# Kernel tuning notes

Hardware: AMD Instinct MI355X
Metric: run time of the kernel (lower is better)

## Reference

```python
import jax, jax.numpy as jnp
import numpy as np

# ---- constants from the source module ----
N_SAMPLES = 2 ** 15          # exp.n_samples
N_FRAMES = 128
N_HARMONICS = 8
N_EVENTS = 8
FILT_SIZE = 16               # freq_domain_filter_size
N_NOTES = 128                # len(scale)
NYQ = 22050.0 / 2.0          # samplerate nyquist
MIN_F0 = 40.0 / NYQ
F0_SPAN = (3000.0 / NYQ) - MIN_F0
MIN_RES = 0.5
RES_SPAN = 1.0 - MIN_RES
B_EVENTS = 128               # batch(16) * n_events(8)

# packed layout (build_param_slices order):
SL_F0 = slice(0, N_NOTES)                       # 0:128
SL_AMP = slice(N_NOTES + N_FRAMES, N_NOTES + 2 * N_FRAMES)   # 256:384
SL_HAMP = slice(N_NOTES + 2 * N_FRAMES, N_NOTES + 2 * N_FRAMES + N_HARMONICS)  # 384:392
SL_HDEC = slice(N_NOTES + 2 * N_FRAMES + N_HARMONICS, N_NOTES + 2 * N_FRAMES + 2 * N_HARMONICS)  # 392:400
SL_FENV = slice(N_NOTES + 2 * N_FRAMES + 2 * N_HARMONICS, N_NOTES + 2 * N_FRAMES + 2 * N_HARMONICS + FILT_SIZE)  # 400:416


def interp_linear(x, out_size):
    """F.interpolate(..., mode='linear', align_corners=False) on last dim of [B,C,L]."""
    L = x.shape[-1]
    scale = L / out_size
    coords = (jnp.arange(out_size, dtype=x.dtype) + 0.5) * scale - 0.5
    coords = jnp.clip(coords, 0.0, L - 1)
    i0 = jnp.floor(coords).astype(jnp.int32)
    i1 = jnp.minimum(i0 + 1, L - 1)
    w = coords - i0.astype(x.dtype)
    return x[..., i0] * (1.0 - w) + x[..., i1] * w


def setup_inputs() -> dict:
    key = jax.random.key(0)
    k1, k2 = jax.random.split(key)
    packed = jax.random.uniform(k1, (B_EVENTS, N_NOTES + 2 * N_FRAMES + 2 * N_HARMONICS + FILT_SIZE), dtype=jnp.float32)
    # musical-scale center frequencies, normalized by nyquist (geometric 20..3000 Hz)
    hz = 20.0 * (3000.0 / 20.0) ** (np.arange(N_NOTES) / (N_NOTES - 1))
    frequencies = jnp.asarray(hz / NYQ, dtype=jnp.float32)
    global_amp = jnp.full((1,), 5000.0, dtype=jnp.float32)
    osc_amp = jnp.full((1,), 50.0, dtype=jnp.float32)
    noise = jax.random.uniform(k2, (B_EVENTS, 1, N_SAMPLES), dtype=jnp.float32, minval=-1.0, maxval=1.0)
    return {"packed": packed, "frequencies": frequencies, "global_amp": global_amp,
            "osc_amp": osc_amp, "noise": noise}


def reference(packed, frequencies, global_amp, osc_amp, noise):
    B = packed.shape[0]
    # ---- f0 (discrete): softmax over notes, expectation, squared, repeated per frame ----
    f0_scalar = jax.nn.softmax(packed[:, SL_F0], axis=-1) @ frequencies          # [B]
    f0 = (f0_scalar ** 2)[:, None, None] * jnp.ones((1, 1, N_FRAMES), packed.dtype)  # [B,1,F]
    f0 = f0 * NYQ
    f0 = MIN_F0 + f0 * F0_SPAN
    # (the torch line `f0 + f0 + f0_fine` has no assignment -> no effect; f0_fine unused)

    # ---- oscillator bank ----
    harm_factors = jnp.arange(1, N_HARMONICS + 1, dtype=packed.dtype)
    osc = f0 * harm_factors[None, :, None]                      # [B,H,F]
    radians = osc / NYQ * jnp.pi
    radians = jnp.where(radians >= jnp.pi, 0.0, radians)
    radians = interp_linear(radians, N_SAMPLES)                  # [B,H,S]
    osc_bank = jnp.sin(jnp.cumsum(radians, axis=-1)) * osc_amp   # [B,H,S]

    # ---- per-harmonic amplitude recurrence (scan over frames) ----
    harm_decay = MIN_RES + packed[:, SL_HDEC] * RES_SPAN         # [B,H]
    harm_amp = packed[:, SL_HAMP]                                # [B,H]
    amp = packed[:, SL_AMP][:, None, :] * 2.0 - 1.0              # [B,1,F]

    def step(current, amp_i):                                    # current [B,H], amp_i [B,1]
        cur = jnp.maximum(current + amp_i * harm_amp, 0.0)       # clamp(0, inf)
        return cur * harm_decay, cur

    amp_frames = jnp.moveaxis(amp[:, 0, :], 1, 0)[:, :, None]    # [F,B,1]
    _, res = jax.lax.scan(step, jnp.zeros((B, N_HARMONICS), packed.dtype), amp_frames)
    res = jnp.moveaxis(res, 0, 2)                                # [B,H,F]
    res_full = interp_linear(res, N_SAMPLES)                     # [B,H,S]

    # ---- FFT-filtered noise ----
    amp_full = interp_linear(amp, N_SAMPLES)                     # [B,1,S]
    nf = packed[:, SL_FENV][:, None, :]                          # [B,1,16]
    nf = interp_linear(nf, N_SAMPLES // 2)
    nf = jnp.pad(nf, ((0, 0), (0, 0), (0, 1)))                   # [B,1,S//2+1]
    noise_scaled = noise * global_amp
    spec = jnp.fft.rfft(noise_scaled, axis=-1, norm='ortho')
    filt = spec * nf
    noise_out = jnp.fft.irfft(filt, n=N_SAMPLES, axis=-1, norm='ortho')
    noise_out = noise_out * jnp.where(amp_full >= 0, amp_full, 0.2 * amp_full)  # leaky_relu(0.2)

    # ---- combine ----
    x = res_full * osc_bank                                      # [B,H,S]
    x = noise_out / N_HARMONICS + x                              # broadcast [B,1,S]
    x = x.reshape(-1, N_EVENTS, N_HARMONICS, N_SAMPLES)
    x = jnp.sum(x, axis=(1, 2)).reshape(-1, 1, N_SAMPLES)        # [batch,1,S]
    return x
```

## Files before the change

### kernel.cpp

```cpp
#include <hip/hip_runtime.h>
#include <math.h>

#define PCK_STRIDE 416
#define N_SAMPLES  32768
#define FFT_M      16384
#define B_EVENTS   128
#define N_GROUPS   16
#define PI_F 3.14159265358979323846f
#define RT2H 0.70710678118654752f

#define MAP(i) ((i) + (((i) >> 5) << 2))
#define LDS_N  18432

__device__ inline float filt_at(const float* __restrict__ f, int k) {
    if (k >= FFT_M) return 0.0f;
    float c = ((float)k + 0.5f) * (1.0f / 1024.0f) - 0.5f;
    c = fminf(fmaxf(c, 0.0f), 15.0f);
    int i0 = (int)floorf(c);
    int i1 = min(i0 + 1, 15);
    float w = c - (float)i0;
    return f[i0] * (1.0f - w) + f[i1] * w;
}

__global__ __launch_bounds__(128) void prep_kernel(
    const float* __restrict__ packed, const float* __restrict__ freqs,
    float* __restrict__ rW, float* __restrict__ res)
{
    const int b = blockIdx.x;
    const int t = threadIdx.x;
    __shared__ float sm[128];
    __shared__ float s_amp[128];
    const float* row = packed + b * PCK_STRIDE;
    float lv = row[t];
    s_amp[t] = row[256 + t] * 2.0f - 1.0f;
    sm[t] = lv; __syncthreads();
    for (int s = 64; s > 0; s >>= 1) { if (t < s) sm[t] = fmaxf(sm[t], sm[t + s]); __syncthreads(); }
    float mx = sm[0]; __syncthreads();
    float ex = __expf(lv - mx);
    sm[t] = ex; __syncthreads();
    for (int s = 64; s > 0; s >>= 1) { if (t < s) sm[t] += sm[t + s]; __syncthreads(); }
    float den = sm[0]; __syncthreads();
    sm[t] = ex * freqs[t]; __syncthreads();
    for (int s = 64; s > 0; s >>= 1) { if (t < s) sm[t] += sm[t + s]; __syncthreads(); }
    float num = sm[0];

    if (t < 8) {
        const float MIN_F0 = 40.0f / 11025.0f;
        const float F0_SPAN = 3000.0f / 11025.0f - 40.0f / 11025.0f;
        float f0s = num / den;
        float f0 = MIN_F0 + f0s * f0s * 11025.0f * F0_SPAN;
        float r = f0 * (float)(t + 1) * (PI_F / 11025.0f);
        if (r >= PI_F) r = 0.0f;
        rW[b * 8 + t] = r;
        float ha = row[384 + t];
        float hd = 0.5f + row[392 + t] * 0.5f;
        float cur = 0.0f;
        float* rr = res + (b * 8 + t) * 128;
        for (int f = 0; f < 128; ++f) {
            float c = fmaxf(cur + s_amp[f] * ha, 0.0f);
            rr[f] = c;
            cur = c * hd;
        }
    }
}

template<int L>
__device__ inline void r4_dif_stage(float* re, float* im, int tid) {
    constexpr int q = L >> 2;
    constexpr float ang = -6.28318530717958647692f / (float)L;
    #pragma unroll 2
    for (int s = 0; s < 8; ++s) {
        int m = tid + (s << 9);
        int t = m & (q - 1);
        int i0 = ((m & ~(q - 1)) << 2) | t;
        int ia = MAP(i0), ib = MAP(i0 + q), ic = MAP(i0 + 2 * q), id = MAP(i0 + 3 * q);
        float ar = re[ia], ai = im[ia];
        float br = re[ib], bi = im[ib];
        float cr = re[ic], ci = im[ic];
        float dr = re[id], di = im[id];
        float s1, c1; __sincosf(ang * (float)t, &s1, &c1);
        float c2 = c1 * c1 - s1 * s1, s2 = 2.0f * c1 * s1;
        float c3 = c2 * c1 - s2 * s1, s3 = c2 * s1 + s2 * c1;
        float s0r = ar + cr, s0i = ai + ci;
        float t1r = br + dr, t1i = bi + di;
        float d0r = ar - cr, d0i = ai - ci;
        float d1r = br - dr, d1i = bi - di;
        re[ia] = s0r + t1r; im[ia] = s0i + t1i;
        float er = s0r - t1r, ei = s0i - t1i;
        re[ib] = er * c2 - ei * s2; im[ib] = er * s2 + ei * c2;
        float fr = d0r + d1i, fi = d0i - d1r;
        re[ic] = fr * c1 - fi * s1; im[ic] = fr * s1 + fi * c1;
        float gr = d0r - d1i, gi = d0i + d1r;
        re[id] = gr * c3 - gi * s3; im[id] = gr * s3 + gi * c3;
    }
    __syncthreads();
}

template<int L>
__device__ inline void r4_dit_stage(float* re, float* im, int tid) {
    constexpr int q = L >> 2;
    constexpr float ang = 6.28318530717958647692f / (float)L;
    #pragma unroll 2
    for (int s = 0; s < 8; ++s) {
        int m = tid + (s << 9);
        int t = m & (q - 1);
        int i0 = ((m & ~(q - 1)) << 2) | t;
        int ia = MAP(i0), ib = MAP(i0 + q), ic = MAP(i0 + 2 * q), id = MAP(i0 + 3 * q);
        float ar = re[ia], ai = im[ia];
        float br = re[ib], bi = im[ib];
        float cr = re[ic], ci = im[ic];
        float dr = re[id], di = im[id];
        float s1, c1; __sincosf(ang * (float)t, &s1, &c1);
        float c2 = c1 * c1 - s1 * s1, s2 = 2.0f * c1 * s1;
        float tbr = br * c2 - bi * s2, tbi = br * s2 + bi * c2;
        float tdr = dr * c2 - di * s2, tdi = dr * s2 + di * c2;
        float B0r = ar + tbr, B0i = ai + tbi;
        float B1r = ar - tbr, B1i = ai - tbi;
        float B2r = cr + tdr, B2i = ci + tdi;
        float B3r = cr - tdr, B3i = ci - tdi;
        float t0r = B2r * c1 - B2i * s1, t0i = B2r * s1 + B2i * c1;
        float t1r = -B3r * s1 - B3i * c1, t1i = B3r * c1 - B3i * s1;
        re[ia] = B0r + t0r; im[ia] = B0i + t0i;
        re[ib] = B1r + t1r; im[ib] = B1i + t1i;
        re[ic] = B0r - t0r; im[ic] = B0i - t0i;
        re[id] = B1r - t1r; im[id] = B1i - t1i;
    }
    __syncthreads();
}

__global__ __launch_bounds__(512)
__attribute__((amdgpu_waves_per_eu(2)))
void fft_filter_kernel(
    const float* __restrict__ noise, const float* __restrict__ packed,
    const float* __restrict__ gamp, float* __restrict__ noise_out)
{
    extern __shared__ float smem[];
    float* re = smem;
    float* im = smem + LDS_N;
    float* filt = smem + 2 * LDS_N;
    const int b = blockIdx.x;
    const int tid = threadIdx.x;
    const float g = gamp[0];

    const float2* nz = (const float2*)(noise + (size_t)b * N_SAMPLES);
    #pragma unroll 4
    for (int s = 0; s < 16; ++s) {
        int j = tid + (s << 9);
        float2 v0 = nz[j];
        float2 v1 = nz[j + 8192];
        float ur = v0.x * g, ui = v0.y * g;
        float wr = v1.x * g, wi = v1.y * g;
        float s1, c1; __sincosf((-PI_F / 8192.0f) * (float)j, &s1, &c1);
        int a0 = MAP(j), a1 = MAP(j + 8192);
        re[a0] = ur + wr; im[a0] = ui + wi;
        float dr = ur - wr, di = ui - wi;
        re[a1] = dr * c1 - di * s1;
        im[a1] = dr * s1 + di * c1;
    }
    if (tid < 16) filt[tid] = packed[b * PCK_STRIDE + 400 + tid];
    __syncthreads();

    r4_dif_stage<8192>(re, im, tid);
    r4_dif_stage<2048>(re, im, tid);
    r4_dif_stage<512>(re, im, tid);
    r4_dif_stage<128>(re, im, tid);
    r4_dif_stage<32>(re, im, tid);

    #pragma unroll 2
    for (int s = 0; s < 4; ++s) {
        int a = 36 * tid + 8 * s;
        float4 r0 = *(const float4*)(re + a);
        float4 r1 = *(const float4*)(re + a + 4);
        float4 q0 = *(const float4*)(im + a);
        float4 q1 = *(const float4*)(im + a + 4);
        float t0r = r0.x + r1.x, t0i = q0.x + q1.x;
        float u0r = r0.x - r1.x, u0i = q0.x - q1.x;
        float d1r = r0.y - r1.y, d1i = q0.y - q1.y;
        float t1r = r0.y + r1.y, t1i = q0.y + q1.y;
        float u1r = RT2H * (d1r + d1i), u1i = RT2H * (d1i - d1r);
        float t2r = r0.z + r1.z, t2i = q0.z + q1.z;
        float d2r = r0.z - r1.z, d2i = q0.z - q1.z;
        float u2r = d2i, u2i = -d2r;
        float t3r = r0.w + r1.w, t3i = q0.w + q1.w;
        float d3r = r0.w - r1.w, d3i = q0.w - q1.w;
        float u3r = RT2H * (d3i - d3r), u3i = -RT2H * (d3r + d3i);
        float A0r = t0r + t2r, A0i = t0i + t2i;
        float A2r = t0r - t2r, A2i = t0i - t2i;
        float A1r = t1r + t3r, A1i = t1i + t3i;
        float e3r = t1r - t3r, e3i = t1i - t3i;
        float A3r = e3i, A3i = -e3r;
        float B0r = u0r + u2r, B0i = u0i + u2i;
        float B2r = u0r - u2r, B2i = u0i - u2i;
        float B1r = u1r + u3r, B1i = u1i + u3i;
        float f3r = u1r - u3r, f3i = u1i - u3i;
        float B3r = f3i, B3i = -f3r;
        r0.x = A0r + A1r; q0.x = A0i + A1i;
        r0.y = A0r - A1r; q0.y = A0i - A1i;
        r0.z = A2r + A3r; q0.z = A2i + A3i;
        r0.w = A2r - A3r; q0.w = A2i - A3i;
        r1.x = B0r + B1r; q1.x = B0i + B1i;
        r1.y = B0r - B1r; q1.y = B0i - B1i;
        r1.z = B2r + B3r; q1.z = B2i + B3i;
        r1.w = B2r - B3r; q1.w = B2i - B3i;
        *(float4*)(re + a) = r0; *(float4*)(re + a + 4) = r1;
        *(float4*)(im + a) = q0; *(float4*)(im + a + 4) = q1;
    }
    __syncthreads();

    const float invM = 1.0f / (float)FFT_M;
    #pragma unroll 2
    for (int s = 0; s < 16; ++s) {
        int jj = (tid + (s << 9)) << 1;
        if (jj == 0) {
            int p0 = MAP(0);
            float z0r = re[p0], z0i = im[p0];
            float y = 0.5f * filt_at(filt, 0) * (z0r + z0i) * invM;
            re[p0] = y; im[p0] = y;
            int p1 = MAP(1);
            float H = filt_at(filt, 8192) * invM;
            re[p1] *= H; im[p1] *= H;
        } else {
            int k = (int)(__brev((unsigned)jj) >> 18);
            int kq = FFT_M - k;
            int pk = MAP(jj);
            int pq = MAP((int)(__brev((unsigned)kq) >> 18));
            float zkr = re[pk], zki = im[pk];
            float zqr = re[pq], zqi = im[pq];
            float Er = 0.5f * (zkr + zqr), Ei = 0.5f * (zki - zqi);
            float Or = 0.5f * (zki + zqi), Oi = 0.5f * (zqr - zkr);
            float th = (float)k * (PI_F / (float)FFT_M);
            float s1, c1; __sincosf(th, &s1, &c1);
            float ts = -s1;
            float tOr = c1 * Or - ts * Oi;
            float tOi = c1 * Oi + ts * Or;
            float Hk = filt_at(filt, k);
            float Hq = filt_at(filt, kq);
            float Ykr = Hk * (Er + tOr), Yki = Hk * (Ei + tOi);
            float Cr  = Hq * (Er - tOr), Ci  = Hq * (Ei - tOi);
            float Ar = 0.5f * (Ykr + Cr), Ai = 0.5f * (Yki + Ci);
            float Br = 0.5f * (Ykr - Cr), Bi = 0.5f * (Yki - Ci);
            re[pk] = (Ar + ts * Br - c1 * Bi) * invM;
            im[pk] = (Ai + c1 * Br + ts * Bi) * invM;
            re[pq] = (Ar + c1 * Bi - ts * Br) * invM;
            im[pq] = (-Ai + c1 * Br + ts * Bi) * invM;
        }
    }
    __syncthreads();

    #pragma unroll 2
    for (int s = 0; s < 4; ++s) {
        int a = 36 * tid + 8 * s;
        float4 r0 = *(const float4*)(re + a);
        float4 r1 = *(const float4*)(re + a + 4);
        float4 q0 = *(const float4*)(im + a);
        float4 q1 = *(const float4*)(im + a + 4);
        float A0r = r0.x + r0.y, A0i = q0.x + q0.y;
        float A1r = r0.x - r0.y, A1i = q0.x - q0.y;
        float A2r = r0.z + r0.w, A2i = q0.z + q0.w;
        float A3r = r0.z - r0.w, A3i = q0.z - q0.w;
        float B0r = r1.x + r1.y, B0i = q1.x + q1.y;
        float B1r = r1.x - r1.y, B1i = q1.x - q1.y;
        float B2r = r1.z + r1.w, B2i = q1.z + q1.w;
        float B3r = r1.z - r1.w, B3i = q1.z - q1.w;
        float t0r = A0r + A2r, t0i = A0i + A2i;
        float t2r = A0r - A2r, t2i = A0i - A2i;
        float w3r = -A3i, w3i = A3r;
        float t1r = A1r + w3r, t1i = A1i + w3i;
        float t3r = A1r - w3r, t3i = A1i - w3i;
        float u0r = B0r + B2r, u0i = B0i + B2i;
        float u2r = B0r - B2r, u2i = B0i - B2i;
        float x3r = -B3i, x3i = B3r;
        float u1r = B1r + x3r, u1i = B1i + x3i;
        float u3r = B1r - x3r, u3i = B1i - x3i;
        float w1r = RT2H * (u1r - u1i), w1i = RT2H * (u1r + u1i);
        float w2r = -u2i,               w2i = u2r;
        float w5r = RT2H * (-u3r - u3i), w5i = RT2H * (u3r - u3i);
        r0.x = t0r + u0r; q0.x = t0i + u0i;
        r1.x = t0r - u0r; q1.x = t0i - u0i;
        r0.y = t1r + w1r; q0.y = t1i + w1i;
        r1.y = t1r - w1r; q1.y = t1i - w1i;
        r0.z = t2r + w2r; q0.z = t2i + w2i;
        r1.z = t2r - w2r; q1.z = t2i - w2i;
        r0.w = t3r + w5r; q0.w = t3i + w5i;
        r1.w = t3r - w5r; q1.w = t3i - w5i;
        *(float4*)(re + a) = r0; *(float4*)(re + a + 4) = r1;
        *(float4*)(im + a) = q0; *(float4*)(im + a + 4) = q1;
    }
    __syncthreads();

    r4_dit_stage<32>(re, im, tid);
    r4_dit_stage<128>(re, im, tid);
    r4_dit_stage<512>(re, im, tid);
    r4_dit_stage<2048>(re, im, tid);
    r4_dit_stage<8192>(re, im, tid);

    float2* oz = (float2*)(noise_out + (size_t)b * N_SAMPLES);
    #pragma unroll 4
    for (int s = 0; s < 16; ++s) {
        int j = tid + (s << 9);
        int a0 = MAP(j), a1 = MAP(j + 8192);
        float ur = re[a0], ui = im[a0];
        float xr = re[a1], xi = im[a1];
        float s1, c1; __sincosf((PI_F / 8192.0f) * (float)j, &s1, &c1);
        float wr = xr * c1 - xi * s1, wi = xr * s1 + xi * c1;
        oz[j] = make_float2(ur + wr, ui + wi);
        oz[j + 8192] = make_float2(ur - wr, ui - wi);
    }
}

__global__ __launch_bounds__(256) void assemble_kernel(
    const float* __restrict__ packed, const float* __restrict__ rW,
    const float* __restrict__ res, const float* __restrict__ noise_out,
    const float* __restrict__ oamp, float* __restrict__ out)
{
    const int g = blockIdx.y;
    const int chunk = blockIdx.x;
    const int tid = threadIdx.x;
    const int n = chunk * 256 + tid;
    const int fb = chunk - 1;

    __shared__ float s_res[8][8][3];
    __shared__ float s_ampf[8][3];
    __shared__ float s_r[8][8];
    if (tid < 192) {
        int e = tid / 24, rem = tid % 24, h = rem / 3, j = rem % 3;
        int f = min(max(fb + j, 0), 127);
        s_res[e][h][j] = res[((g * 8 + e) * 8 + h) * 128 + f];
    }
    if (tid < 24) {
        int e = tid / 3, j = tid % 3;
        int f = min(max(fb + j, 0), 127);
        s_ampf[e][j] = packed[(g * 8 + e) * PCK_STRIDE + 256 + f] * 2.0f - 1.0f;
    }
    if (tid >= 192 && tid < 256) {
        int u = tid - 192;
        s_r[u / 8][u % 8] = rW[g * 64 + u];
    }
    __syncthreads();

    float coords = ((float)n + 0.5f) * (1.0f / 256.0f) - 0.5f;
    coords = fminf(fmaxf(coords, 0.0f), 127.0f);
    int i0 = (int)floorf(coords);
    float w = coords - (float)i0;
    int j0 = i0 - fb;
    float osc50 = oamp[0];
    float pn = (float)(n + 1);
    float wm = 1.0f - w;

    float acc = 0.0f;
    #pragma unroll
    for (int e = 0; e < 8; ++e) {
        int b = g * 8 + e;
        float nv = noise_out[(size_t)b * N_SAMPLES + n];
        float av = s_ampf[e][j0] * wm + s_ampf[e][j0 + 1] * w;
        float gate = (av >= 0.0f) ? av : 0.2f * av;
        acc += nv * gate;
        float sn, cn; __sincosf(pn * s_r[e][0], &sn, &cn);
        float c2 = 2.0f * cn;
        float shm1 = 0.0f, sh = sn;
        #pragma unroll
        for (int h = 0; h < 8; ++h) {
            float rsv = s_res[e][h][j0] * wm + s_res[e][h][j0 + 1] * w;
            float sv = (s_r[e][h] != 0.0f) ? sh : 0.0f;
            acc += rsv * osc50 * sv;
            float nx = c2 * sh - shm1;
            shm1 = sh; sh = nx;
        }
    }
    out[(size_t)g * N_SAMPLES + n] = acc;
}

extern "C" void kernel_launch(void* const* d_in, const int* in_sizes, int n_in,
                              void* d_out, int out_size, void* d_ws, size_t ws_size,
                              hipStream_t stream) {
    const float* packed = (const float*)d_in[0];
    const float* freqs  = (const float*)d_in[1];
    const float* gamp   = (const float*)d_in[2];
    const float* oamp   = (const float*)d_in[3];
    const float* noise  = (const float*)d_in[4];
    float* out = (float*)d_out;

    float* ws = (float*)d_ws;
    float* noise_out = ws;
    float* res = ws + (size_t)B_EVENTS * N_SAMPLES;
    float* rW  = res + B_EVENTS * 8 * 128;

    prep_kernel<<<B_EVENTS, 128, 0, stream>>>(packed, freqs, rW, res);
    fft_filter_kernel<<<B_EVENTS, 512, (2 * LDS_N + 16) * sizeof(float), stream>>>(
        noise, packed, gamp, noise_out);
    assemble_kernel<<<dim3(N_SAMPLES / 256, N_GROUPS), 256, 0, stream>>>(
        packed, rW, res, noise_out, oamp, out);
}
```

Before: 120.4 us.

## Fuse prep into FFT kernel and double FFT block threads to 1024

Removes the separate prep kernel by computing the softmax f0 and the resonance recurrence inside the FFT kernel, using a single wavefront with shuffle reductions while other threads load noise. The FFT block grows from 512 to 1024 threads, with the per-thread loop counts and the radix-8 indexing adjusted to match, to raise the number of waves in flight per block. The cost is one fewer launch and more parallelism per FFT, in exchange for higher register pressure at 1024 threads and a serial 128-step recurrence that lengthens the critical path before the first barrier.

```diff
diff --git a/kernel.cpp b/kernel.cpp
--- a/kernel.cpp
+++ b/kernel.cpp
@@ -6,6 +6,7 @@
 #define FFT_M      16384
 #define B_EVENTS   128
 #define N_GROUPS   16
+#define NT         1024
 #define PI_F 3.14159265358979323846f
 #define RT2H 0.70710678118654752f
 
@@ -22,55 +23,13 @@
     return f[i0] * (1.0f - w) + f[i1] * w;
 }
 
-__global__ __launch_bounds__(128) void prep_kernel(
-    const float* __restrict__ packed, const float* __restrict__ freqs,
-    float* __restrict__ rW, float* __restrict__ res)
-{
-    const int b = blockIdx.x;
-    const int t = threadIdx.x;
-    __shared__ float sm[128];
-    __shared__ float s_amp[128];
-    const float* row = packed + b * PCK_STRIDE;
-    float lv = row[t];
-    s_amp[t] = row[256 + t] * 2.0f - 1.0f;
-    sm[t] = lv; __syncthreads();
-    for (int s = 64; s > 0; s >>= 1) { if (t < s) sm[t] = fmaxf(sm[t], sm[t + s]); __syncthreads(); }
-    float mx = sm[0]; __syncthreads();
-    float ex = __expf(lv - mx);
-    sm[t] = ex; __syncthreads();
-    for (int s = 64; s > 0; s >>= 1) { if (t < s) sm[t] += sm[t + s]; __syncthreads(); }
-    float den = sm[0]; __syncthreads();
-    sm[t] = ex * freqs[t]; __syncthreads();
-    for (int s = 64; s > 0; s >>= 1) { if (t < s) sm[t] += sm[t + s]; __syncthreads(); }
-    float num = sm[0];
-
-    if (t < 8) {
-        const float MIN_F0 = 40.0f / 11025.0f;
-        const float F0_SPAN = 3000.0f / 11025.0f - 40.0f / 11025.0f;
-        float f0s = num / den;
-        float f0 = MIN_F0 + f0s * f0s * 11025.0f * F0_SPAN;
-        float r = f0 * (float)(t + 1) * (PI_F / 11025.0f);
-        if (r >= PI_F) r = 0.0f;
-        rW[b * 8 + t] = r;
-        float ha = row[384 + t];
-        float hd = 0.5f + row[392 + t] * 0.5f;
-        float cur = 0.0f;
-        float* rr = res + (b * 8 + t) * 128;
-        for (int f = 0; f < 128; ++f) {
-            float c = fmaxf(cur + s_amp[f] * ha, 0.0f);
-            rr[f] = c;
-            cur = c * hd;
-        }
-    }
-}
-
 template<int L>
 __device__ inline void r4_dif_stage(float* re, float* im, int tid) {
     constexpr int q = L >> 2;
     constexpr float ang = -6.28318530717958647692f / (float)L;
     #pragma unroll 2
-    for (int s = 0; s < 8; ++s) {
-        int m = tid + (s << 9);
+    for (int s = 0; s < (FFT_M / 4) / NT; ++s) {
+        int m = tid + s * NT;
         int t = m & (q - 1);
         int i0 = ((m & ~(q - 1)) << 2) | t;
         int ia = MAP(i0), ib = MAP(i0 + q), ic = MAP(i0 + 2 * q), id = MAP(i0 + 3 * q);
@@ -101,8 +60,8 @@
     constexpr int q = L >> 2;
     constexpr float ang = 6.28318530717958647692f / (float)L;
     #pragma unroll 2
-    for (int s = 0; s < 8; ++s) {
-        int m = tid + (s << 9);
+    for (int s = 0; s < (FFT_M / 4) / NT; ++s) {
+        int m = tid + s * NT;
         int t = m & (q - 1);
         int i0 = ((m & ~(q - 1)) << 2) | t;
         int ia = MAP(i0), ib = MAP(i0 + q), ic = MAP(i0 + 2 * q), id = MAP(i0 + 3 * q);
@@ -128,11 +87,11 @@
     __syncthreads();
 }
 
-__global__ __launch_bounds__(512)
-__attribute__((amdgpu_waves_per_eu(2)))
+__global__ __launch_bounds__(NT)
 void fft_filter_kernel(
     const float* __restrict__ noise, const float* __restrict__ packed,
-    const float* __restrict__ gamp, float* __restrict__ noise_out)
+    const float* __restrict__ gamp, float* __restrict__ noise_out,
+    const float* __restrict__ freqs, float* __restrict__ rW, float* __restrict__ res)
 {
     extern __shared__ float smem[];
     float* re = smem;
@@ -144,8 +103,8 @@
 
     const float2* nz = (const float2*)(noise + (size_t)b * N_SAMPLES);
     #pragma unroll 4
-    for (int s = 0; s < 16; ++s) {
-        int j = tid + (s << 9);
+    for (int s = 0; s < 8192 / NT; ++s) {
+        int j = tid + s * NT;
         float2 v0 = nz[j];
         float2 v1 = nz[j + 8192];
         float ur = v0.x * g, ui = v0.y * g;
@@ -157,7 +116,49 @@
         re[a1] = dr * c1 - di * s1;
         im[a1] = dr * s1 + di * c1;
     }
-    if (tid < 16) filt[tid] = packed[b * PCK_STRIDE + 400 + tid];
+    if (tid >= 64 && tid < 80) filt[tid - 64] = packed[b * PCK_STRIDE + 400 + (tid - 64)];
+
+    if (tid < 64) {
+        const float* row = packed + b * PCK_STRIDE;
+        float n0 = row[tid], n1 = row[tid + 64];
+        float fq0 = freqs[tid], fq1 = freqs[tid + 64];
+        float mx = fmaxf(n0, n1);
+        #pragma unroll
+        for (int off = 32; off >= 1; off >>= 1) mx = fmaxf(mx, __shfl_xor(mx, off));
+        float e0 = __expf(n0 - mx), e1 = __expf(n1 - mx);
+        float den = e0 + e1, num = e0 * fq0 + e1 * fq1;
+        #pragma unroll
+        for (int off = 32; off >= 1; off >>= 1) {
+            den += __shfl_xor(den, off);
+            num += __shfl_xor(num, off);
+        }
+        float ampA = row[256 + tid] * 2.0f - 1.0f;
+        float ampB = row[320 + tid] * 2.0f - 1.0f;
+        int h = tid & 7;
+        float ha = row[384 + h];
+        float hd = 0.5f + row[392 + h] * 0.5f;
+        const float MIN_F0 = 40.0f / 11025.0f;
+        const float F0_SPAN = 3000.0f / 11025.0f - 40.0f / 11025.0f;
+        float f0s = num / den;
+        float f0 = MIN_F0 + f0s * f0s * 11025.0f * F0_SPAN;
+        float r = f0 * (float)(h + 1) * (PI_F / 11025.0f);
+        if (r >= PI_F) r = 0.0f;
+        if (tid < 8) rW[b * 8 + tid] = r;
+        float cur = 0.0f;
+        float* rr = res + (b * 8 + h) * 128;
+        for (int f = 0; f < 64; ++f) {
+            float av = __shfl(ampA, f);
+            float c = fmaxf(cur + av * ha, 0.0f);
+            if (tid < 8) rr[f] = c;
+            cur = c * hd;
+        }
+        for (int f = 0; f < 64; ++f) {
+            float av = __shfl(ampB, f);
+            float c = fmaxf(cur + av * ha, 0.0f);
+            if (tid < 8) rr[64 + f] = c;
+            cur = c * hd;
+        }
+    }
     __syncthreads();
 
     r4_dif_stage<8192>(re, im, tid);
@@ -167,8 +168,10 @@
     r4_dif_stage<32>(re, im, tid);
 
     #pragma unroll 2
-    for (int s = 0; s < 4; ++s) {
-        int a = 36 * tid + 8 * s;
+    for (int s = 0; s < 2048 / NT; ++s) {
+        int m = (NT / 512) * tid + s;
+        int i = 8 * m;
+        int a = MAP(i);
         float4 r0 = *(const float4*)(re + a);
         float4 r1 = *(const float4*)(re + a + 4);
         float4 q0 = *(const float4*)(im + a);
@@ -209,8 +212,8 @@
 
     const float invM = 1.0f / (float)FFT_M;
     #pragma unroll 2
-    for (int s = 0; s < 16; ++s) {
-        int jj = (tid + (s << 9)) << 1;
+    for (int s = 0; s < 8192 / NT; ++s) {
+        int jj = (tid + s * NT) << 1;
         if (jj == 0) {
             int p0 = MAP(0);
             float z0r = re[p0], z0i = im[p0];
@@ -248,8 +251,9 @@
     __syncthreads();
 
     #pragma unroll 2
-    for (int s = 0; s < 4; ++s) {
-        int a = 36 * tid + 8 * s;
+    for (int s = 0; s < 2048 / NT; ++s) {
+        int m = (NT / 512) * tid + s;
+        int a = MAP(8 * m);
         float4 r0 = *(const float4*)(re + a);
         float4 r1 = *(const float4*)(re + a + 4);
         float4 q0 = *(const float4*)(im + a);
@@ -296,8 +300,8 @@
 
     float2* oz = (float2*)(noise_out + (size_t)b * N_SAMPLES);
     #pragma unroll 4
-    for (int s = 0; s < 16; ++s) {
-        int j = tid + (s << 9);
+    for (int s = 0; s < 8192 / NT; ++s) {
+        int j = tid + s * NT;
         int a0 = MAP(j), a1 = MAP(j + 8192);
         float ur = re[a0], ui = im[a0];
         float xr = re[a1], xi = im[a1];
@@ -385,9 +389,8 @@
     float* res = ws + (size_t)B_EVENTS * N_SAMPLES;
     float* rW  = res + B_EVENTS * 8 * 128;
 
-    prep_kernel<<<B_EVENTS, 128, 0, stream>>>(packed, freqs, rW, res);
-    fft_filter_kernel<<<B_EVENTS, 512, (2 * LDS_N + 16) * sizeof(float), stream>>>(
-        noise, packed, gamp, noise_out);
+    fft_filter_kernel<<<B_EVENTS, NT, (2 * LDS_N + 16) * sizeof(float), stream>>>(
+        noise, packed, gamp, noise_out, freqs, rW, res);
     assemble_kernel<<<dim3(N_SAMPLES / 256, N_GROUPS), 256, 0, stream>>>(
         packed, rW, res, noise_out, oamp, out);
 }
```

Result: slower. 129.8 us (+7.8%).
